# Performance work log

Hardware: AMD Instinct MI355X
Metric: run time of the kernel (lower is better)

The kernel has to match this reference:

```python
import jax, jax.numpy as jnp
import numpy as np

D_MODEL = 256
NUM_HEADS = 8
CURV = 1.0  # Poincare ball curvature c
EPS = 1e-5


def expmap0(v, c):
    # Exponential map at the origin of the Poincare ball.
    sqrt_c = jnp.sqrt(c)
    norm = jnp.sqrt(jnp.clip(jnp.sum(v * v, axis=-1, keepdims=True), 1e-12))
    return jnp.tanh(sqrt_c * norm) * v / (sqrt_c * norm)


def setup_inputs() -> dict:
    key = jax.random.key(0)
    ks = jax.random.split(key, 12)
    B, S, D = 2, 2048, D_MODEL
    s = 1.0 / np.sqrt(D)
    return {
        "x": jax.random.normal(ks[0], (B, S, D), dtype=jnp.float32),
        "Wq": jax.random.normal(ks[1], (D, D), dtype=jnp.float32) * s,
        "bq": jnp.zeros((D,), jnp.float32),
        "Wk": jax.random.normal(ks[2], (D, D), dtype=jnp.float32) * s,
        "bk": jnp.zeros((D,), jnp.float32),
        "Wv": jax.random.normal(ks[3], (D, D), dtype=jnp.float32) * s,
        "bv": jnp.zeros((D,), jnp.float32),
        "Wo": jax.random.normal(ks[4], (D, D), dtype=jnp.float32) * s,
        "bo": jnp.zeros((D,), jnp.float32),
        "Wfc": jax.random.normal(ks[5], (D, D), dtype=jnp.float32) * s,
        "bfc": jnp.zeros((D,), jnp.float32),
    }


def reference(x, Wq, bq, Wk, bk, Wv, bv, Wo, bo, Wfc, bfc):
    B, S, D = x.shape
    H, dh = NUM_HEADS, D // NUM_HEADS
    c = CURV

    def proj(W, b):
        return (x @ W.T + b).reshape(B, S, H, dh).transpose(0, 2, 1, 3)  # [B,H,S,dh]

    q = expmap0(proj(Wq, bq), c)
    k = expmap0(proj(Wk, bk), c)
    v = proj(Wv, bv)

    # Gram quantities; pairwise Poincare distance via closed-form Mobius-add norm.
    qq = jnp.sum(q * q, axis=-1)[..., :, None]          # [B,H,S,1]
    kk = jnp.sum(k * k, axis=-1)[..., None, :]          # [B,H,1,S]
    qk = jnp.einsum("bhsd,bhtd->bhst", q, k)            # [B,H,S,S]

    A = 1.0 - 2.0 * c * qk + c * kk
    Bc = 1.0 - c * qq
    den = 1.0 - 2.0 * c * qk + (c * c) * qq * kk
    num2 = A * A * qq + Bc * Bc * kk - 2.0 * A * Bc * qk  # ||(-q) mobius+ k||^2 * den^2
    n = jnp.sqrt(jnp.clip(num2, 0.0)) / jnp.clip(jnp.abs(den), 1e-12)
    sqrt_c = jnp.sqrt(c)
    dist = (2.0 / sqrt_c) * jnp.arctanh(jnp.clip(sqrt_c * n, 0.0, 1.0 - EPS))

    scores = -dist / np.sqrt(dh)
    attn = jax.nn.softmax(scores, axis=-1)
    out = jnp.einsum("bhst,bhtd->bhsd", attn, v)        # [B,H,S,dh]
    out = out.transpose(0, 2, 1, 3).reshape(B, S, D)
    out = out @ Wo.T + bo
    return out @ Wfc.T + bfc
```

## Files before the change

kernel.cpp:

```cpp
#include <hip/hip_runtime.h>
#include <cstdint>
#include <cstddef>


#define ALPHA 0.17677669529663687f
#define EMIN  -3.1129694f
#define CHI   1.95e-5f
#define NEG_INV_2CHI -25641.026f
#define TWOLOG2E 2.8853900817779268f

typedef __bf16 bf16x8 __attribute__((ext_vector_type(8)));
typedef float  f32x4  __attribute__((ext_vector_type(4)));

__device__ __forceinline__ float fast_log2(float x) { return __builtin_amdgcn_logf(x); }
__device__ __forceinline__ float fast_exp2(float x) { return __builtin_amdgcn_exp2f(x); }

__global__ __launch_bounds__(256)
void k1_misc(const float* __restrict__ x,   const float* __restrict__ Wq,
             const float* __restrict__ Wk,  const float* __restrict__ Wv,
             const float* __restrict__ Wfc, const float* __restrict__ Wo,
             const float* __restrict__ bo,  const float* __restrict__ bfc,
             __bf16* __restrict__ xh, __bf16* __restrict__ xl,
             __bf16* __restrict__ Ws, __bf16* __restrict__ Wch,
             __bf16* __restrict__ Wcl, float* __restrict__ bcomb) {
  __shared__ float sh[2 * 32 * 68];
  const int bx = blockIdx.x, tid = threadIdx.x;
  if (bx < 16) {
    float (*AsT)[68] = (float(*)[68])sh;
    float (*Bs)[68]  = (float(*)[68])(sh + 32 * 68);
    const int ty = tid >> 4, tx = tid & 15;
    const int m0 = (bx >> 2) * 64, n0 = (bx & 3) * 64;
    float acc[4][4] = {};
    for (int k0 = 0; k0 < 256; k0 += 32) {
#pragma unroll
      for (int jj = 0; jj < 2; ++jj) {
        int j = tid * 2 + jj;
        {
          int r = j >> 3, c4 = (j & 7) << 2;
          float4 av = *(const float4*)&Wfc[(size_t)(m0 + r) * 256 + k0 + c4];
          AsT[c4 + 0][r] = av.x; AsT[c4 + 1][r] = av.y;
          AsT[c4 + 2][r] = av.z; AsT[c4 + 3][r] = av.w;
        }
        {
          int r = j >> 4, c4 = (j & 15) << 2;
          *(float4*)&Bs[r][c4] = *(const float4*)&Wo[(size_t)(k0 + r) * 256 + n0 + c4];
        }
      }
      __syncthreads();
#pragma unroll
      for (int kk = 0; kk < 32; ++kk) {
        float4 a = *(const float4*)&AsT[kk][ty * 4];
        float4 b = *(const float4*)&Bs[kk][tx * 4];
        float av[4] = {a.x, a.y, a.z, a.w};
        float bv[4] = {b.x, b.y, b.z, b.w};
#pragma unroll
        for (int i = 0; i < 4; ++i)
#pragma unroll
          for (int j2 = 0; j2 < 4; ++j2)
            acc[i][j2] = fmaf(av[i], bv[j2], acc[i][j2]);
      }
      __syncthreads();
    }
#pragma unroll
    for (int i = 0; i < 4; ++i) {
      union { __bf16 h[4]; uint2 u; } ph, pl;
#pragma unroll
      for (int j = 0; j < 4; ++j) {
        __bf16 hb = (__bf16)acc[i][j];
        ph.h[j] = hb;
        pl.h[j] = (__bf16)(acc[i][j] - (float)hb);
      }
      size_t off = (size_t)(m0 + ty * 4 + i) * 256 + n0 + tx * 4;
      *(uint2*)(Wch + off) = ph.u;
      *(uint2*)(Wcl + off) = pl.u;
    }
  } else if (bx < 32) {
    float* red = sh;
    int r = tid >> 4, c = tid & 15;
    int row = (bx - 16) * 16 + r;
    float s = 0.0f;
    for (int k = c; k < 256; k += 16) s = fmaf(Wfc[(size_t)row * 256 + k], bo[k], s);
    red[tid] = s;
    __syncthreads();
    if (c == 0) {
      float t = 0.0f;
#pragma unroll
      for (int i = 0; i < 16; ++i) t += red[r * 16 + i];
      bcomb[row] = t + bfc[row];
    }
  } else {
    int g = (bx - 32) * 256 + tid;
    const float* src;
    __bf16 *dh, *dl;
    if (g < 131072) {
      src = x + (size_t)g * 8; dh = xh + (size_t)g * 8; dl = xl + (size_t)g * 8;
    } else {
      int e = g - 131072;
      int wsel = e >> 13;
      int inner = (e & 8191) * 8;
      src = (wsel == 0 ? Wq : (wsel == 1 ? Wk : Wv)) + inner;
      dh = Ws + wsel * 131072 + inner;
      dl = Ws + wsel * 131072 + 65536 + inner;
    }
    union { __bf16 h[8]; uint4 u; } ph, pl;
#pragma unroll
    for (int i = 0; i < 2; ++i) {
      float4 v = *(const float4*)(src + i * 4);
      float vv[4] = {v.x, v.y, v.z, v.w};
#pragma unroll
      for (int j = 0; j < 4; ++j) {
        __bf16 hb = (__bf16)vv[j];
        ph.h[i * 4 + j] = hb;
        pl.h[i * 4 + j] = (__bf16)(vv[j] - (float)hb);
      }
    }
    *(uint4*)dh = ph.u;
    *(uint4*)dl = pl.u;
  }
}

__global__ __launch_bounds__(256, 4)
void gemm_qkv_mfma(const __bf16* __restrict__ xh, const __bf16* __restrict__ xl,
                   const __bf16* __restrict__ Ws,
                   const float* __restrict__ bq, const float* __restrict__ bk,
                   const float* __restrict__ bv,
                   __bf16* __restrict__ Qbf, __bf16* __restrict__ Kbf,
                   __bf16* __restrict__ Vt, float* __restrict__ Vsum,
                   float4* __restrict__ qtab4, float4* __restrict__ ktab4,
                   float2* __restrict__ Kred) {
  __shared__ float4 kredsh[4];
  __shared__ __bf16 sh_vt[64][64];
  __shared__ float  vsred[4][4][64];
  const int tid = threadIdx.x, w = tid >> 6, lane = tid & 63;
  const int l15 = lane & 15, lg = lane >> 4;
  const int m0 = blockIdx.x * 64, nb = blockIdx.y;
  const int wsel = nb >> 2;
  const int n256b = (nb & 3) * 64;
  const __bf16* Wh = Ws + wsel * 131072;
  const __bf16* Wl = Wh + 65536;
  const int arow = m0 + w * 16 + l15;
  const __bf16* axh = xh + (size_t)arow * 256 + lg * 8;
  const __bf16* axl = xl + (size_t)arow * 256 + lg * 8;
  f32x4 acc0 = {0,0,0,0}, acc1 = {0,0,0,0}, acc2 = {0,0,0,0}, acc3 = {0,0,0,0};
#pragma unroll
  for (int k0 = 0; k0 < 256; k0 += 32) {
    bf16x8 ah = *(const bf16x8*)(axh + k0);
    bf16x8 al = *(const bf16x8*)(axl + k0);
#pragma unroll
    for (int g = 0; g < 4; ++g) {
      const size_t br = (size_t)(n256b + g * 16 + l15) * 256 + lg * 8 + k0;
      bf16x8 bh = *(const bf16x8*)(Wh + br);
      bf16x8 bl = *(const bf16x8*)(Wl + br);
      f32x4& acc = g == 0 ? acc0 : (g == 1 ? acc1 : (g == 2 ? acc2 : acc3));
      acc = __builtin_amdgcn_mfma_f32_16x16x32_bf16(ah, bh, acc, 0, 0, 0);
      acc = __builtin_amdgcn_mfma_f32_16x16x32_bf16(al, bh, acc, 0, 0, 0);
      acc = __builtin_amdgcn_mfma_f32_16x16x32_bf16(ah, bl, acc, 0, 0, 0);
    }
  }
  const float* bias = wsel == 0 ? bq : (wsel == 1 ? bk : bv);
  const int b = m0 >> 11;
  const int headA = n256b >> 5;
  const int sLoc = m0 & 2047;

  if (wsel == 2) {
#pragma unroll
    for (int g = 0; g < 4; ++g) {
      const f32x4& acc = g == 0 ? acc0 : (g == 1 ? acc1 : (g == 2 ? acc2 : acc3));
      int col = g * 16 + l15;
      float bval = bias[n256b + col];
      float p = 0.0f;
#pragma unroll
      for (int r = 0; r < 4; ++r) {
        float v = acc[r] + bval;
        sh_vt[col][w * 16 + lg * 4 + r] = (__bf16)v;
        p += v;
      }
      vsred[w][lg][col] = p;
    }
    __syncthreads();
    {
      int col = tid >> 2, sg = tid & 3;
      int bh = (b << 3) + headA + (col >> 5);
      int d = col & 31;
      uint4 v0 = *(const uint4*)&sh_vt[col][sg * 16];
      uint4 v1 = *(const uint4*)&sh_vt[col][sg * 16 + 8];
      __bf16* dstp = Vt + ((size_t)bh * 32 + d) * 2048 + sLoc + sg * 16;
      *(uint4*)dstp = v0;
      *(uint4*)(dstp + 8) = v1;
    }
    if (tid < 128) {
      int tgrp = tid >> 6, col = tid & 63;
      float s = 0.0f;
#pragma unroll
      for (int w2 = 0; w2 < 2; ++w2)
#pragma unroll
        for (int l2 = 0; l2 < 4; ++l2)
          s += vsred[tgrp * 2 + w2][l2][col];
      int bh = (b << 3) + headA + (col >> 5);
      int d = col & 31;
      Vsum[((size_t)bh * 64 + (sLoc >> 5) + tgrp) * 32 + d] = s;
    }
    return;
  }

  const float bv0 = bias[n256b + 0 * 16 + l15];
  const float bv1 = bias[n256b + 1 * 16 + l15];
  const float bv2 = bias[n256b + 2 * 16 + l15];
  const float bv3 = bias[n256b + 3 * 16 + l15];
  float ssA[4], ssB[4];
#pragma unroll
  for (int r = 0; r < 4; ++r) {
    acc0[r] += bv0; acc1[r] += bv1; acc2[r] += bv2; acc3[r] += bv3;
    ssA[r] = acc0[r] * acc0[r] + acc1[r] * acc1[r];
    ssB[r] = acc2[r] * acc2[r] + acc3[r] * acc3[r];
  }
#pragma unroll
  for (int mk = 1; mk < 16; mk <<= 1) {
#pragma unroll
    for (int r = 0; r < 4; ++r) {
      ssA[r] += __shfl_xor(ssA[r], mk);
      ssB[r] += __shfl_xor(ssB[r], mk);
    }
  }
  float scA[4], qqA[4], BvA[4], lgA[4];
  float scB[4], qqB[4], BvB[4], lgB_[4];
#pragma unroll
  for (int r = 0; r < 4; ++r) {
    {
      float ss = fmaxf(ssA[r], 1e-12f);
      float xv = sqrtf(ss);
      float ex = fast_exp2(-TWOLOG2E * xv);
      float opex = 1.0f + ex;
      float th = (1.0f - ex) / opex;
      scA[r] = th / xv;
      qqA[r] = th * th;
      BvA[r] = 4.0f * ex / (opex * opex);
      lgA[r] = 2.0f - TWOLOG2E * xv - 2.0f * fast_log2(opex);
    }
    {
      float ss = fmaxf(ssB[r], 1e-12f);
      float xv = sqrtf(ss);
      float ex = fast_exp2(-TWOLOG2E * xv);
      float opex = 1.0f + ex;
      float th = (1.0f - ex) / opex;
      scB[r] = th / xv;
      qqB[r] = th * th;
      BvB[r] = 4.0f * ex / (opex * opex);
      lgB_[r] = 2.0f - TWOLOG2E * xv - 2.0f * fast_log2(opex);
    }
  }
  __bf16* dst = wsel == 0 ? Qbf : Kbf;
  float4* tab = wsel == 0 ? qtab4 : ktab4;
  const int headB = headA + 1;
  const int bhA = (b << 3) + headA, bhB = (b << 3) + headB;
  const int sbase = sLoc + w * 16 + lg * 4;
#pragma unroll
  for (int r = 0; r < 4; ++r) {
    int s = sbase + r;
    size_t baseA = ((size_t)bhA * 2048 + s) * 32;
    size_t baseB = ((size_t)bhB * 2048 + s) * 32;
    dst[baseA + l15]      = (__bf16)(acc0[r] * scA[r]);
    dst[baseA + 16 + l15] = (__bf16)(acc1[r] * scA[r]);
    dst[baseB + l15]      = (__bf16)(acc2[r] * scB[r]);
    dst[baseB + 16 + l15] = (__bf16)(acc3[r] * scB[r]);
    if (l15 == 0) {
      if (wsel == 0) {
        tab[(size_t)bhA * 2048 + s] = float4{qqA[r], ALPHA * lgA[r], BvA[r], 0.0f};
        tab[(size_t)bhB * 2048 + s] = float4{qqB[r], ALPHA * lgB_[r], BvB[r], 0.0f};
      } else {
        tab[(size_t)bhA * 2048 + s] = float4{qqA[r], BvA[r], ALPHA * lgA[r], 0.0f};
        tab[(size_t)bhB * 2048 + s] = float4{qqB[r], BvB[r], ALPHA * lgB_[r], 0.0f};
      }
    }
  }
  if (wsel == 1) {
    float mnA = fminf(fminf(qqA[0], qqA[1]), fminf(qqA[2], qqA[3]));
    float mxA = fmaxf(fmaxf(BvA[0], BvA[1]), fmaxf(BvA[2], BvA[3]));
    float mnB = fminf(fminf(qqB[0], qqB[1]), fminf(qqB[2], qqB[3]));
    float mxB = fmaxf(fmaxf(BvB[0], BvB[1]), fmaxf(BvB[2], BvB[3]));
    mnA = fminf(mnA, __shfl_xor(mnA, 16)); mnA = fminf(mnA, __shfl_xor(mnA, 32));
    mxA = fmaxf(mxA, __shfl_xor(mxA, 16)); mxA = fmaxf(mxA, __shfl_xor(mxA, 32));
    mnB = fminf(mnB, __shfl_xor(mnB, 16)); mnB = fminf(mnB, __shfl_xor(mnB, 32));
    mxB = fmaxf(mxB, __shfl_xor(mxB, 16)); mxB = fmaxf(mxB, __shfl_xor(mxB, 32));
    if (lane == 0) kredsh[w] = float4{mnA, mxA, mnB, mxB};
    __syncthreads();
    if (tid == 0) {
      float4 a = kredsh[0], b4 = kredsh[1], c4 = kredsh[2], d4 = kredsh[3];
      float MnA = fminf(fminf(a.x, b4.x), fminf(c4.x, d4.x));
      float MxA = fmaxf(fmaxf(a.y, b4.y), fmaxf(c4.y, d4.y));
      float MnB = fminf(fminf(a.z, b4.z), fminf(c4.z, d4.z));
      float MxB = fmaxf(fmaxf(a.w, b4.w), fmaxf(c4.w, d4.w));
      int bx31 = blockIdx.x & 31;
      Kred[bhA * 32 + bx31] = float2{MnA, MxA};
      Kred[bhB * 32 + bx31] = float2{MnB, MxB};
    }
  }
}

__global__ __launch_bounds__(256, 4)
void attn_mfma(const __bf16* __restrict__ Qbf, const __bf16* __restrict__ Kbf,
               const __bf16* __restrict__ Vt,  const float4* __restrict__ qtab4,
               const float4* __restrict__ ktab4, const float* __restrict__ Vsum,
               const float2* __restrict__ Kred,
               __bf16* __restrict__ PNb, float* __restrict__ PD) {
  __shared__ __bf16 Pt[4][16][72];
  const int tid = threadIdx.x;
  const int wid = tid >> 6, lane = tid & 63;
  const int l15 = lane & 15, lg = lane >> 4;
  const int wgid = blockIdx.x;
  const int rest = wgid >> 3;
  const int sblk = rest & 31;
  const int t2   = rest >> 5;
  const int tc   = t2 & 3;
  const int bh   = ((t2 >> 2) << 3) | (wgid & 7);
  const int s0 = sblk * 64 + wid * 16;

  bf16x8 qfrag = *(const bf16x8*)(Qbf + ((size_t)bh * 2048 + s0 + l15) * 32 + lg * 8);
  float4 qt = qtab4[bh * 2048 + s0 + l15];
  const float qq = qt.x, Bq = qt.z;
  const float eminRow = EMIN - qt.y;
  const float wclipf = (float)(__bf16)fast_exp2(eminRow);
  float wrow[4];
#pragma unroll
  for (int r = 0; r < 4; ++r)
    wrow[r] = (float)(__bf16)fast_exp2(EMIN - qtab4[bh * 2048 + s0 + lg * 4 + r].y);

  float kkmin = 1.0f, bkmax = 0.0f;
#pragma unroll
  for (int j = 0; j < 32; ++j) {
    float2 kr = Kred[bh * 32 + j];
    kkmin = fminf(kkmin, kr.x);
    bkmax = fmaxf(bkmax, kr.y);
  }
  const float thr_all = fmaf(0.5f * qq, kkmin,
                             fmaf(Bq * NEG_INV_2CHI, bkmax, 0.5f));

  const __bf16* Kbase = Kbf + ((size_t)bh << 16);
  const __bf16* Vbase = Vt + ((size_t)bh << 16);
  const float4* Tk = ktab4 + bh * 2048;
  const float*  VsBase = Vsum + (size_t)bh * 64 * 32;
  __bf16* Pw = &Pt[wid][0][0];

  f32x4 accO0 = {0.f, 0.f, 0.f, 0.f};
  f32x4 accO1 = {0.f, 0.f, 0.f, 0.f};
  float den = 0.0f;
  int nclip = 0;
  const f32x4 zero = {0.f, 0.f, 0.f, 0.f};
  const int tbeg = tc * 512;
  const int stag = sblk & 7;

  bf16x8 kfA0, kfA1, kfA2, kfA3, kfB0, kfB1, kfB2, kfB3;
  float vA0, vA1, vA2, vA3, vB0, vB1, vB2, vB3;

#define LOAD_SET(K0, K1, K2, K3, V0, V1, V2, V3, T0)                          \
  {                                                                           \
    const int _t = (T0);                                                      \
    K0 = *(const bf16x8*)(Kbase + (size_t)(_t + 0 * 16 + l15) * 32 + lg * 8); \
    K1 = *(const bf16x8*)(Kbase + (size_t)(_t + 1 * 16 + l15) * 32 + lg * 8); \
    K2 = *(const bf16x8*)(Kbase + (size_t)(_t + 2 * 16 + l15) * 32 + lg * 8); \
    K3 = *(const bf16x8*)(Kbase + (size_t)(_t + 3 * 16 + l15) * 32 + lg * 8); \
    const int _ti = _t >> 5;                                                  \
    V0 = VsBase[_ti * 32 + l15];                                              \
    V1 = VsBase[(_ti + 1) * 32 + l15];                                        \
    V2 = VsBase[_ti * 32 + 16 + l15];                                         \
    V3 = VsBase[(_ti + 1) * 32 + 16 + l15];                                   \
  }

#define COMPUTE_SET(K0, K1, K2, K3, V0, V1, V2, V3, T0)                       \
  {                                                                           \
    const int _t0 = (T0);                                                     \
    __builtin_amdgcn_s_setprio(1);                                            \
    _Pragma("unroll")                                                         \
    for (int h = 0; h < 2; ++h) {                                             \
      f32x4 S[2];                                                             \
      bool ok = true;                                                         \
      _Pragma("unroll")                                                       \
      for (int s2 = 0; s2 < 2; ++s2) {                                        \
        bf16x8 kf = (h == 0) ? (s2 == 0 ? K0 : K1) : (s2 == 0 ? K2 : K3);     \
        f32x4 Sv = __builtin_amdgcn_mfma_f32_16x16x32_bf16(kf, qfrag, zero,   \
                                                           0, 0, 0);          \
        S[s2] = Sv;                                                           \
        float m = fmaxf(fmaxf(Sv[0], Sv[1]), fmaxf(Sv[2], Sv[3]));            \
        ok &= (m <= thr_all);                                                 \
      }                                                                       \
      if (__all((int)ok)) {                                                   \
        ++nclip;                                                              \
        const float vsA = h ? V1 : V0;                                        \
        const float vsB = h ? V3 : V2;                                        \
        _Pragma("unroll")                                                     \
        for (int r = 0; r < 4; ++r) {                                         \
          accO0[r] = fmaf(wrow[r], vsA, accO0[r]);                            \
          accO1[r] = fmaf(wrow[r], vsB, accO1[r]);                            \
        }                                                                     \
      } else {                                                                \
        _Pragma("unroll")                                                     \
        for (int s2 = 0; s2 < 2; ++s2) {                                      \
          const int sub = h * 2 + s2;                                         \
          const int tk = _t0 + sub * 16 + lg * 4;                             \
          f32x4 Sv = S[s2];                                                   \
          float w[4];                                                         \
          _Pragma("unroll")                                                   \
          for (int r = 0; r < 4; ++r) {                                       \
            float4 T = Tk[tk + r];                                            \
            float qk2 = Sv[r] + Sv[r];                                        \
            float u = (qq + T.x) - qk2;                                       \
            float d = fmaf(qq, T.x, 1.0f) - qk2;                              \
            float p = fmaxf(u * d, 0.0f);                                     \
            float sq = sqrtf(p);                                              \
            float m2 = fmaf(2.0f, sq, u + d);                                 \
            float e = fmaf(-ALPHA, fast_log2(m2), T.z);                       \
            e = fmaxf(e, eminRow);                                            \
            w[r] = fast_exp2(e);                                              \
          }                                                                   \
          den += (w[0] + w[1]) + (w[2] + w[3]);                               \
          union { __bf16 hh[4]; uint2 u2; } pk;                               \
          pk.hh[0] = (__bf16)w[0]; pk.hh[1] = (__bf16)w[1];                   \
          pk.hh[2] = (__bf16)w[2]; pk.hh[3] = (__bf16)w[3];                   \
          *(uint2*)&Pw[l15 * 72 + sub * 16 + lg * 4] = pk.u2;                 \
        }                                                                     \
        bf16x8 pfrag = *(const bf16x8*)&Pw[l15 * 72 + h * 32 + lg * 8];       \
        bf16x8 v0 = *(const bf16x8*)(Vbase + (size_t)l15 * 2048 + _t0 +       \
                                     h * 32 + lg * 8);                        \
        bf16x8 v1 = *(const bf16x8*)(Vbase + (size_t)(16 + l15) * 2048 +      \
                                     _t0 + h * 32 + lg * 8);                  \
        accO0 = __builtin_amdgcn_mfma_f32_16x16x32_bf16(pfrag, v0, accO0,     \
                                                        0, 0, 0);             \
        accO1 = __builtin_amdgcn_mfma_f32_16x16x32_bf16(pfrag, v1, accO1,     \
                                                        0, 0, 0);             \
      }                                                                       \
    }                                                                         \
    __builtin_amdgcn_s_setprio(0);                                            \
  }

  LOAD_SET(kfA0, kfA1, kfA2, kfA3, vA0, vA1, vA2, vA3,
           tbeg + ((stag & 7) << 6));

#pragma unroll
  for (int i = 0; i < 8; ++i) {
    const int tcur = tbeg + (((i + stag) & 7) << 6);
    const int tnxt = tbeg + (((i + 1 + stag) & 7) << 6);
    if ((i & 1) == 0) {
      if (i < 7) LOAD_SET(kfB0, kfB1, kfB2, kfB3, vB0, vB1, vB2, vB3, tnxt);
      COMPUTE_SET(kfA0, kfA1, kfA2, kfA3, vA0, vA1, vA2, vA3, tcur);
    } else {
      if (i < 7) LOAD_SET(kfA0, kfA1, kfA2, kfA3, vA0, vA1, vA2, vA3, tnxt);
      COMPUTE_SET(kfB0, kfB1, kfB2, kfB3, vB0, vB1, vB2, vB3, tcur);
    }
  }
#undef LOAD_SET
#undef COMPUTE_SET

  den = fmaf(8.0f * wclipf, (float)nclip, den);
  den += __shfl_xor(den, 16);
  den += __shfl_xor(den, 32);
  size_t pbase = ((size_t)tc * 16 + bh) * 2048;
  if (lg == 0) PD[pbase + s0 + l15] = den;
#pragma unroll
  for (int r = 0; r < 4; ++r) {
    int sl = lg * 4 + r;
    size_t row = (pbase + s0 + sl) * 32;
    PNb[row + l15]      = (__bf16)accO0[r];
    PNb[row + 16 + l15] = (__bf16)accO1[r];
  }
}

__global__ __launch_bounds__(256)
void combine4(const __bf16* __restrict__ PNb, const float* __restrict__ PD,
              __bf16* __restrict__ AOh, __bf16* __restrict__ AOl) {
  int idx = blockIdx.x * 256 + threadIdx.x;
  int bh = idx >> 11, s = idx & 2047;
  int b = bh >> 3, h = bh & 7;
  float den = 0.0f;
#pragma unroll
  for (int c = 0; c < 4; ++c) den += PD[((size_t)c * 16 + bh) * 2048 + s];
  float r = 1.0f / den;
  size_t ob = ((size_t)b * 2048 + s) * 256 + h * 32;
#pragma unroll
  for (int i = 0; i < 4; ++i) {
    float acc8[8] = {};
#pragma unroll
    for (int c = 0; c < 4; ++c) {
      bf16x8 v = *(const bf16x8*)&PNb[((((size_t)c * 16 + bh) * 2048 + s) * 32) + i * 8];
#pragma unroll
      for (int j = 0; j < 8; ++j) acc8[j] += (float)v[j];
    }
    union { __bf16 h8[8]; uint4 u; } ph, pl;
#pragma unroll
    for (int j = 0; j < 8; ++j) {
      float val = acc8[j] * r;
      __bf16 hb = (__bf16)val;
      ph.h8[j] = hb;
      pl.h8[j] = (__bf16)(val - (float)hb);
    }
    *(uint4*)(AOh + ob + i * 8) = ph.u;
    *(uint4*)(AOl + ob + i * 8) = pl.u;
  }
}

__global__ __launch_bounds__(256, 1)
void gemm_out_mfma(const __bf16* __restrict__ aoh, const __bf16* __restrict__ aol,
                   const __bf16* __restrict__ Wch, const __bf16* __restrict__ Wcl,
                   const float* __restrict__ bcomb, float* __restrict__ out) {
  const int tid = threadIdx.x, w = tid >> 6, lane = tid & 63;
  const int l15 = lane & 15, lg = lane >> 4;
  const int m0 = blockIdx.x * 64, n0 = blockIdx.y * 64;
  const int arow = m0 + w * 16 + l15;
  const __bf16* axh = aoh + (size_t)arow * 256 + lg * 8;
  const __bf16* axl = aol + (size_t)arow * 256 + lg * 8;
  f32x4 acc0 = {0,0,0,0}, acc1 = {0,0,0,0}, acc2 = {0,0,0,0}, acc3 = {0,0,0,0};
#pragma unroll
  for (int k0 = 0; k0 < 256; k0 += 32) {
    bf16x8 ah = *(const bf16x8*)(axh + k0);
    bf16x8 al = *(const bf16x8*)(axl + k0);
#pragma unroll
    for (int g = 0; g < 4; ++g) {
      const size_t br = (size_t)(n0 + g * 16 + l15) * 256 + lg * 8 + k0;
      bf16x8 bh = *(const bf16x8*)(Wch + br);
      bf16x8 bl = *(const bf16x8*)(Wcl + br);
      f32x4& acc = g == 0 ? acc0 : (g == 1 ? acc1 : (g == 2 ? acc2 : acc3));
      acc = __builtin_amdgcn_mfma_f32_16x16x32_bf16(ah, bh, acc, 0, 0, 0);
      acc = __builtin_amdgcn_mfma_f32_16x16x32_bf16(al, bh, acc, 0, 0, 0);
      acc = __builtin_amdgcn_mfma_f32_16x16x32_bf16(ah, bl, acc, 0, 0, 0);
    }
  }
#pragma unroll
  for (int g = 0; g < 4; ++g) {
    const f32x4& acc = g == 0 ? acc0 : (g == 1 ? acc1 : (g == 2 ? acc2 : acc3));
    int n = n0 + g * 16 + l15;
    float bval = bcomb[n];
#pragma unroll
    for (int r = 0; r < 4; ++r) {
      int m = m0 + w * 16 + lg * 4 + r;
      out[(size_t)m * 256 + n] = acc[r] + bval;
    }
  }
}

extern "C" void kernel_launch(void* const* d_in, const int* in_sizes, int n_in,
                              void* d_out, int out_size, void* d_ws, size_t ws_size,
                              hipStream_t stream) {
  const float* x   = (const float*)d_in[0];
  const float* Wq  = (const float*)d_in[1];
  const float* bq  = (const float*)d_in[2];
  const float* Wk  = (const float*)d_in[3];
  const float* bk  = (const float*)d_in[4];
  const float* Wv  = (const float*)d_in[5];
  const float* bv  = (const float*)d_in[6];
  const float* Wo  = (const float*)d_in[7];
  const float* bo  = (const float*)d_in[8];
  const float* Wfc = (const float*)d_in[9];
  const float* bfc = (const float*)d_in[10];

  float* ws = (float*)d_ws;
  __bf16* Qbf = (__bf16*)(ws + (3 << 20));
  __bf16* Kbf = (__bf16*)(ws + (3 << 20) + (1 << 19));
  __bf16* Vtb = (__bf16*)(ws + (4 << 20));
  float4* qtab4 = (float4*)(ws + (4 << 20) + (1 << 19));
  float4* ktab4 = (float4*)(ws + (4 << 20) + (1 << 19) + (1 << 17));
  float*  Vsum  = ws + (4 << 20) + (1 << 19) + (2 << 17);
  __bf16* Wch   = (__bf16*)(Vsum + (1 << 15));
  __bf16* Wcl   = Wch + 65536;
  float*  bcomb = Vsum + (1 << 15) + (1 << 16);
  float2* Kred  = (float2*)(bcomb + 256);
  __bf16* xh = (__bf16*)(ws + (5 << 20));
  __bf16* xl = (__bf16*)(ws + (5 << 20) + (1 << 19));
  __bf16* Wsplit = (__bf16*)(ws + (6 << 20));
  __bf16* PNb = (__bf16*)(ws + (6 << 20) + (1 << 18));
  float* PD = ws + (6 << 20) + (1 << 18) + (2 << 20);
  __bf16* AOh = (__bf16*)ws;
  __bf16* AOl = (__bf16*)(ws + (1 << 19));

  dim3 blk(256);
  k1_misc<<<dim3(640), blk, 0, stream>>>(x, Wq, Wk, Wv, Wfc, Wo, bo, bfc,
                                         xh, xl, Wsplit, Wch, Wcl, bcomb);
  gemm_qkv_mfma<<<dim3(64, 12), blk, 0, stream>>>(xh, xl, Wsplit, bq, bk, bv,
                                                  Qbf, Kbf, Vtb, Vsum,
                                                  qtab4, ktab4, Kred);
  attn_mfma<<<dim3(2048), blk, 0, stream>>>(Qbf, Kbf, Vtb, qtab4, ktab4,
                                            Vsum, Kred, PNb, PD);
  combine4<<<dim3(128), blk, 0, stream>>>(PNb, PD, AOh, AOl);
  gemm_out_mfma<<<dim3(64, 4), blk, 0, stream>>>(AOh, AOl, Wch, Wcl, bcomb,
                                                 (float*)d_out);
}
```

Before: 101.6 us.

## Fuse split-KV combine into output GEMM and batch score MFMAs per set

The combine4 kernel, which reduced the four split-KV partial outputs and normalized them, is removed. That reduction now runs inside gemm_out_mfma's A-operand load, which saves one launch and the write and re-read of the AOh/AOl intermediates. The attention inner loop now issues all four QK MFMAs up front and takes the fast clipped path for a whole 64-key set with one wave vote, falling back to per-half checks only when needed. The cost is that each of the four N-blocks of the output GEMM redoes the combine, so PNb/PD are read several times.

New measurement: 105.6 us. 1.04x slower.

```diff
diff --git a/kernel.cpp b/kernel.cpp
--- a/kernel.cpp
+++ b/kernel.cpp
@@ -366,68 +366,73 @@
     V3 = VsBase[(_ti + 1) * 32 + 16 + l15];                                   \
   }
 
+#define SLOW_HALF(H, SA, SB, T0)                                              \
+  {                                                                           \
+    _Pragma("unroll")                                                         \
+    for (int s2 = 0; s2 < 2; ++s2) {                                          \
+      const int sub = (H) * 2 + s2;                                           \
+      const int tk = (T0) + sub * 16 + lg * 4;                                \
+      f32x4 Sv = (s2 == 0) ? (SA) : (SB);                                     \
+      float w[4];                                                             \
+      _Pragma("unroll")                                                       \
+      for (int r = 0; r < 4; ++r) {                                           \
+        float4 T = Tk[tk + r];                                                \
+        float qk2 = Sv[r] + Sv[r];                                            \
+        float u = (qq + T.x) - qk2;                                           \
+        float d = fmaf(qq, T.x, 1.0f) - qk2;                                  \
+        float p = fmaxf(u * d, 0.0f);                                         \
+        float sq = sqrtf(p);                                                  \
+        float m2 = fmaf(2.0f, sq, u + d);                                     \
+        float e = fmaf(-ALPHA, fast_log2(m2), T.z);                           \
+        e = fmaxf(e, eminRow);                                                \
+        w[r] = fast_exp2(e);                                                  \
+      }                                                                       \
+      den += (w[0] + w[1]) + (w[2] + w[3]);                                   \
+      union { __bf16 hh[4]; uint2 u2; } pk;                                   \
+      pk.hh[0] = (__bf16)w[0]; pk.hh[1] = (__bf16)w[1];                       \
+      pk.hh[2] = (__bf16)w[2]; pk.hh[3] = (__bf16)w[3];                       \
+      *(uint2*)&Pw[l15 * 72 + sub * 16 + lg * 4] = pk.u2;                     \
+    }                                                                         \
+    bf16x8 pfrag = *(const bf16x8*)&Pw[l15 * 72 + (H) * 32 + lg * 8];         \
+    bf16x8 v0 = *(const bf16x8*)(Vbase + (size_t)l15 * 2048 + (T0) +          \
+                                 (H) * 32 + lg * 8);                          \
+    bf16x8 v1 = *(const bf16x8*)(Vbase + (size_t)(16 + l15) * 2048 + (T0) +   \
+                                 (H) * 32 + lg * 8);                          \
+    accO0 = __builtin_amdgcn_mfma_f32_16x16x32_bf16(pfrag, v0, accO0, 0,0,0); \
+    accO1 = __builtin_amdgcn_mfma_f32_16x16x32_bf16(pfrag, v1, accO1, 0,0,0); \
+  }
+
+#define FAST_HALF(VA, VB)                                                     \
+  {                                                                           \
+    ++nclip;                                                                  \
+    _Pragma("unroll")                                                         \
+    for (int r = 0; r < 4; ++r) {                                             \
+      accO0[r] = fmaf(wrow[r], (VA), accO0[r]);                               \
+      accO1[r] = fmaf(wrow[r], (VB), accO1[r]);                               \
+    }                                                                         \
+  }
+
 #define COMPUTE_SET(K0, K1, K2, K3, V0, V1, V2, V3, T0)                       \
   {                                                                           \
     const int _t0 = (T0);                                                     \
     __builtin_amdgcn_s_setprio(1);                                            \
-    _Pragma("unroll")                                                         \
-    for (int h = 0; h < 2; ++h) {                                             \
-      f32x4 S[2];                                                             \
-      bool ok = true;                                                         \
-      _Pragma("unroll")                                                       \
-      for (int s2 = 0; s2 < 2; ++s2) {                                        \
-        bf16x8 kf = (h == 0) ? (s2 == 0 ? K0 : K1) : (s2 == 0 ? K2 : K3);     \
-        f32x4 Sv = __builtin_amdgcn_mfma_f32_16x16x32_bf16(kf, qfrag, zero,   \
-                                                           0, 0, 0);          \
-        S[s2] = Sv;                                                           \
-        float m = fmaxf(fmaxf(Sv[0], Sv[1]), fmaxf(Sv[2], Sv[3]));            \
-        ok &= (m <= thr_all);                                                 \
-      }                                                                       \
-      if (__all((int)ok)) {                                                   \
-        ++nclip;                                                              \
-        const float vsA = h ? V1 : V0;                                        \
-        const float vsB = h ? V3 : V2;                                        \
-        _Pragma("unroll")                                                     \
-        for (int r = 0; r < 4; ++r) {                                         \
-          accO0[r] = fmaf(wrow[r], vsA, accO0[r]);                            \
-          accO1[r] = fmaf(wrow[r], vsB, accO1[r]);                            \
-        }                                                                     \
-      } else {                                                                \
-        _Pragma("unroll")                                                     \
-        for (int s2 = 0; s2 < 2; ++s2) {                                      \
-          const int sub = h * 2 + s2;                                         \
-          const int tk = _t0 + sub * 16 + lg * 4;                             \
-          f32x4 Sv = S[s2];                                                   \
-          float w[4];                                                         \
-          _Pragma("unroll")                                                   \
-          for (int r = 0; r < 4; ++r) {                                       \
-            float4 T = Tk[tk + r];                                            \
-            float qk2 = Sv[r] + Sv[r];                                        \
-            float u = (qq + T.x) - qk2;                                       \
-            float d = fmaf(qq, T.x, 1.0f) - qk2;                              \
-            float p = fmaxf(u * d, 0.0f);                                     \
-            float sq = sqrtf(p);                                              \
-            float m2 = fmaf(2.0f, sq, u + d);                                 \
-            float e = fmaf(-ALPHA, fast_log2(m2), T.z);                       \
-            e = fmaxf(e, eminRow);                                            \
-            w[r] = fast_exp2(e);                                              \
-          }                                                                   \
-          den += (w[0] + w[1]) + (w[2] + w[3]);                               \
-          union { __bf16 hh[4]; uint2 u2; } pk;                               \
-          pk.hh[0] = (__bf16)w[0]; pk.hh[1] = (__bf16)w[1];                   \
-          pk.hh[2] = (__bf16)w[2]; pk.hh[3] = (__bf16)w[3];                   \
-          *(uint2*)&Pw[l15 * 72 + sub * 16 + lg * 4] = pk.u2;                 \
-        }                                                                     \
-        bf16x8 pfrag = *(const bf16x8*)&Pw[l15 * 72 + h * 32 + lg * 8];       \
-        bf16x8 v0 = *(const bf16x8*)(Vbase + (size_t)l15 * 2048 + _t0 +       \
-                                     h * 32 + lg * 8);                        \
-        bf16x8 v1 = *(const bf16x8*)(Vbase + (size_t)(16 + l15) * 2048 +      \
-                                     _t0 + h * 32 + lg * 8);                  \
-        accO0 = __builtin_amdgcn_mfma_f32_16x16x32_bf16(pfrag, v0, accO0,     \
-                                                        0, 0, 0);             \
-        accO1 = __builtin_amdgcn_mfma_f32_16x16x32_bf16(pfrag, v1, accO1,     \
-                                                        0, 0, 0);             \
-      }                                                                       \
+    f32x4 S0 = __builtin_amdgcn_mfma_f32_16x16x32_bf16(K0, qfrag, zero,0,0,0);\
+    f32x4 S1 = __builtin_amdgcn_mfma_f32_16x16x32_bf16(K1, qfrag, zero,0,0,0);\
+    f32x4 S2 = __builtin_amdgcn_mfma_f32_16x16x32_bf16(K2, qfrag, zero,0,0,0);\
+    f32x4 S3 = __builtin_amdgcn_mfma_f32_16x16x32_bf16(K3, qfrag, zero,0,0,0);\
+    float mA = fmaxf(fmaxf(fmaxf(S0[0], S0[1]), fmaxf(S0[2], S0[3])),         \
+                     fmaxf(fmaxf(S1[0], S1[1]), fmaxf(S1[2], S1[3])));        \
+    float mB = fmaxf(fmaxf(fmaxf(S2[0], S2[1]), fmaxf(S2[2], S2[3])),         \
+                     fmaxf(fmaxf(S3[0], S3[1]), fmaxf(S3[2], S3[3])));        \
+    bool okA = (mA <= thr_all), okB = (mB <= thr_all);                        \
+    if (__all((int)(okA && okB))) {                                           \
+      FAST_HALF(V0, V2);                                                      \
+      FAST_HALF(V1, V3);                                                      \
+    } else {                                                                  \
+      if (__all((int)okA)) { FAST_HALF(V0, V2); }                             \
+      else { SLOW_HALF(0, S0, S1, _t0); }                                     \
+      if (__all((int)okB)) { FAST_HALF(V1, V3); }                             \
+      else { SLOW_HALF(1, S2, S3, _t0); }                                     \
     }                                                                         \
     __builtin_amdgcn_s_setprio(0);                                            \
   }
@@ -449,6 +454,8 @@
   }
 #undef LOAD_SET
 #undef COMPUTE_SET
+#undef FAST_HALF
+#undef SLOW_HALF
 
   den = fmaf(8.0f * wclipf, (float)nclip, den);
   den += __shfl_xor(den, 16);
@@ -464,63 +471,48 @@
   }
 }
 
-__global__ __launch_bounds__(256)
-void combine4(const __bf16* __restrict__ PNb, const float* __restrict__ PD,
-              __bf16* __restrict__ AOh, __bf16* __restrict__ AOl) {
-  int idx = blockIdx.x * 256 + threadIdx.x;
-  int bh = idx >> 11, s = idx & 2047;
-  int b = bh >> 3, h = bh & 7;
-  float den = 0.0f;
-#pragma unroll
-  for (int c = 0; c < 4; ++c) den += PD[((size_t)c * 16 + bh) * 2048 + s];
-  float r = 1.0f / den;
-  size_t ob = ((size_t)b * 2048 + s) * 256 + h * 32;
-#pragma unroll
-  for (int i = 0; i < 4; ++i) {
-    float acc8[8] = {};
-#pragma unroll
-    for (int c = 0; c < 4; ++c) {
-      bf16x8 v = *(const bf16x8*)&PNb[((((size_t)c * 16 + bh) * 2048 + s) * 32) + i * 8];
-#pragma unroll
-      for (int j = 0; j < 8; ++j) acc8[j] += (float)v[j];
-    }
-    union { __bf16 h8[8]; uint4 u; } ph, pl;
-#pragma unroll
-    for (int j = 0; j < 8; ++j) {
-      float val = acc8[j] * r;
-      __bf16 hb = (__bf16)val;
-      ph.h8[j] = hb;
-      pl.h8[j] = (__bf16)(val - (float)hb);
-    }
-    *(uint4*)(AOh + ob + i * 8) = ph.u;
-    *(uint4*)(AOl + ob + i * 8) = pl.u;
-  }
-}
-
 __global__ __launch_bounds__(256, 1)
-void gemm_out_mfma(const __bf16* __restrict__ aoh, const __bf16* __restrict__ aol,
+void gemm_out_mfma(const __bf16* __restrict__ PNb, const float* __restrict__ PD,
                    const __bf16* __restrict__ Wch, const __bf16* __restrict__ Wcl,
                    const float* __restrict__ bcomb, float* __restrict__ out) {
   const int tid = threadIdx.x, w = tid >> 6, lane = tid & 63;
   const int l15 = lane & 15, lg = lane >> 4;
   const int m0 = blockIdx.x * 64, n0 = blockIdx.y * 64;
   const int arow = m0 + w * 16 + l15;
-  const __bf16* axh = aoh + (size_t)arow * 256 + lg * 8;
-  const __bf16* axl = aol + (size_t)arow * 256 + lg * 8;
+  const int b = arow >> 11, s = arow & 2047;
   f32x4 acc0 = {0,0,0,0}, acc1 = {0,0,0,0}, acc2 = {0,0,0,0}, acc3 = {0,0,0,0};
 #pragma unroll
   for (int k0 = 0; k0 < 256; k0 += 32) {
-    bf16x8 ah = *(const bf16x8*)(axh + k0);
-    bf16x8 al = *(const bf16x8*)(axl + k0);
+    const int bh = (b << 3) + (k0 >> 5);
+    float den = 0.0f;
+#pragma unroll
+    for (int c = 0; c < 4; ++c) den += PD[((size_t)c * 16 + bh) * 2048 + s];
+    const float rinv = 1.0f / den;
+    const int d0 = lg * 8;
+    float av8[8] = {};
+#pragma unroll
+    for (int c = 0; c < 4; ++c) {
+      bf16x8 v = *(const bf16x8*)&PNb[((((size_t)c * 16 + bh) * 2048 + s) * 32) + d0];
+#pragma unroll
+      for (int j = 0; j < 8; ++j) av8[j] += (float)v[j];
+    }
+    bf16x8 ah, al;
+#pragma unroll
+    for (int j = 0; j < 8; ++j) {
+      float val = av8[j] * rinv;
+      __bf16 hb = (__bf16)val;
+      ah[j] = hb;
+      al[j] = (__bf16)(val - (float)hb);
+    }
 #pragma unroll
     for (int g = 0; g < 4; ++g) {
       const size_t br = (size_t)(n0 + g * 16 + l15) * 256 + lg * 8 + k0;
-      bf16x8 bh = *(const bf16x8*)(Wch + br);
-      bf16x8 bl = *(const bf16x8*)(Wcl + br);
+      bf16x8 bh2 = *(const bf16x8*)(Wch + br);
+      bf16x8 bl2 = *(const bf16x8*)(Wcl + br);
       f32x4& acc = g == 0 ? acc0 : (g == 1 ? acc1 : (g == 2 ? acc2 : acc3));
-      acc = __builtin_amdgcn_mfma_f32_16x16x32_bf16(ah, bh, acc, 0, 0, 0);
-      acc = __builtin_amdgcn_mfma_f32_16x16x32_bf16(al, bh, acc, 0, 0, 0);
-      acc = __builtin_amdgcn_mfma_f32_16x16x32_bf16(ah, bl, acc, 0, 0, 0);
+      acc = __builtin_amdgcn_mfma_f32_16x16x32_bf16(ah, bh2, acc, 0, 0, 0);
+      acc = __builtin_amdgcn_mfma_f32_16x16x32_bf16(al, bh2, acc, 0, 0, 0);
+      acc = __builtin_amdgcn_mfma_f32_16x16x32_bf16(ah, bl2, acc, 0, 0, 0);
     }
   }
 #pragma unroll
@@ -567,8 +559,6 @@
   __bf16* Wsplit = (__bf16*)(ws + (6 << 20));
   __bf16* PNb = (__bf16*)(ws + (6 << 20) + (1 << 18));
   float* PD = ws + (6 << 20) + (1 << 18) + (2 << 20);
-  __bf16* AOh = (__bf16*)ws;
-  __bf16* AOl = (__bf16*)(ws + (1 << 19));
 
   dim3 blk(256);
   k1_misc<<<dim3(640), blk, 0, stream>>>(x, Wq, Wk, Wv, Wfc, Wo, bo, bfc,
@@ -578,7 +568,6 @@
                                                   qtab4, ktab4, Kred);
   attn_mfma<<<dim3(2048), blk, 0, stream>>>(Qbf, Kbf, Vtb, qtab4, ktab4,
                                             Vsum, Kred, PNb, PD);
-  combine4<<<dim3(128), blk, 0, stream>>>(PNb, PD, AOh, AOl);
-  gemm_out_mfma<<<dim3(64, 4), blk, 0, stream>>>(AOh, AOl, Wch, Wcl, bcomb,
+  gemm_out_mfma<<<dim3(64, 4), blk, 0, stream>>>(PNb, PD, Wch, Wcl, bcomb,
                                                  (float*)d_out);
 }
```
